# Performance work log

Measured on AMD Instinct MI355X. Metric: run time of the kernel, lower is better.

Reference implementation:

```python
import jax, jax.numpy as jnp
import numpy as np

S = 2048        # tokens (single prefill sequence)
HID = 3584      # hidden_size
H = 16          # num query heads
KV = 8          # num kv heads
D = 256         # head_dim
WINDOW = 1024   # sliding window size
CAP = 50.0      # logit softcap
SCALE = 256.0 ** -0.5   # query_pre_attn_scalar ** -0.5
THETA = 10000.0


def setup_inputs() -> dict:
    key = jax.random.key(0)
    ks = jax.random.split(key, 5)
    hidden_states = jax.random.normal(ks[0], (S, HID), dtype=jnp.float32)
    positions = jnp.arange(S, dtype=jnp.int32)
    Wq = jax.random.normal(ks[1], (HID, H * D), dtype=jnp.float32) * 0.02
    Wk = jax.random.normal(ks[2], (HID, KV * D), dtype=jnp.float32) * 0.02
    Wv = jax.random.normal(ks[3], (HID, KV * D), dtype=jnp.float32) * 0.02
    Wo = jax.random.normal(ks[4], (H * D, HID), dtype=jnp.float32) * 0.02
    return {"hidden_states": hidden_states, "positions": positions,
            "Wq": Wq, "Wk": Wk, "Wv": Wv, "Wo": Wo}


def _rope_neox(x, positions):
    # x: [S, n_heads, D]; neox-style: rotate halves, full rotary_dim == D
    half = D // 2
    inv_freq = 1.0 / (THETA ** (jnp.arange(0, half, dtype=jnp.float32) * 2.0 / D))
    freqs = positions.astype(jnp.float32)[:, None] * inv_freq[None, :]  # [S, half]
    cos = jnp.cos(freqs)[:, None, :].astype(x.dtype)
    sin = jnp.sin(freqs)[:, None, :].astype(x.dtype)
    x1, x2 = x[..., :half], x[..., half:]
    return jnp.concatenate([x1 * cos - x2 * sin, x2 * cos + x1 * sin], axis=-1)


def reference(hidden_states, positions, Wq, Wk, Wv, Wo):
    # QKV projections (no bias)
    q = (hidden_states @ Wq).reshape(S, H, D)
    k = (hidden_states @ Wk).reshape(S, KV, D)
    v = (hidden_states @ Wv).reshape(S, KV, D)
    q = _rope_neox(q, positions)
    k = _rope_neox(k, positions)
    # grouped-query attention: G query heads per kv head
    G = H // KV
    qg = q.reshape(S, KV, G, D)
    scores = jnp.einsum('qkgd,skd->kgqs', qg, k) * jnp.asarray(SCALE, q.dtype)
    # logit soft-capping
    scores = CAP * jnp.tanh(scores / CAP)
    # causal + sliding-window mask
    i = positions[:, None]
    j = positions[None, :]
    mask = (j <= i) & ((i - j) < WINDOW)   # [S, S]
    neg = jnp.finfo(scores.dtype).min
    scores = jnp.where(mask[None, None, :, :], scores, neg)
    p = jax.nn.softmax(scores, axis=-1)
    attn = jnp.einsum('kgqs,skd->qkgd', p, v).reshape(S, H * D)
    return attn @ Wo
```

## Files before the change

### kernel.cpp

```cpp
#include <hip/hip_runtime.h>
#include <stdint.h>

#define S 2048
#define HID 3584
#define NH 16
#define NKV 8
#define DH 256
#define WINDOW 1024
#define SCALE 0.0625f
#define CAP 50.0f

typedef short s16x8 __attribute__((ext_vector_type(8)));
typedef float f32x4 __attribute__((ext_vector_type(4)));

__device__ __forceinline__ short f2bf(float f) {
  union { float f; uint32_t u; } c; c.f = f;
  uint32_t u = c.u;
  uint32_t r = (u + 0x7FFFu + ((u >> 16) & 1u)) >> 16;
  return (short)r;
}
__device__ __forceinline__ float bf2f(short s) {
  union { uint32_t u; float f; } c;
  c.u = ((uint32_t)(uint16_t)s) << 16;
  return c.f;
}
__device__ __forceinline__ void gll16(const void* g, void* l) {
  __builtin_amdgcn_global_load_lds((const __attribute__((address_space(1))) void*)g,
                                   (__attribute__((address_space(3))) void*)l, 16, 0, 0);
}
#define BAR() asm volatile("s_barrier" ::: "memory")
#define VW6() asm volatile("s_waitcnt vmcnt(6)" ::: "memory")

__global__ void rope_table_kernel(float2* __restrict__ tbl) {
  int idx = blockIdx.x * 256 + threadIdx.x;
  int s = idx >> 7, i = idx & 127;
  float inv = __expf(-(float)i * (9.210340371976184f / 128.0f));
  float fr = (float)s * inv;
  tbl[idx] = make_float2(cosf(fr), sinf(fr));
}

__global__ void conv_hs_kernel(const float* __restrict__ src, short* __restrict__ dst) {
  int gid = blockIdx.x * 256 + threadIdx.x;
  float4 a = *(const float4*)&src[(size_t)gid * 8];
  float4 b = *(const float4*)&src[(size_t)gid * 8 + 4];
  s16x8 o;
  o[0] = f2bf(a.x); o[1] = f2bf(a.y); o[2] = f2bf(a.z); o[3] = f2bf(a.w);
  o[4] = f2bf(b.x); o[5] = f2bf(b.y); o[6] = f2bf(b.z); o[7] = f2bf(b.w);
  *(s16x8*)&dst[(size_t)gid * 8] = o;
}

__global__ __launch_bounds__(256)
void transpose_kernel(const float* __restrict__ src, short* __restrict__ dst,
                      int K, int N)
{
  __shared__ __align__(16) short t[64][76];
  int ntn = N >> 6;
  int tn = blockIdx.x % ntn, tk = blockIdx.x / ntn;
  int tid = threadIdx.x;
  int c = tid & 63, rg = tid >> 6;
  #pragma unroll
  for (int i = 0; i < 4; ++i) {
    int r0 = i * 16 + rg * 4;
    short tmp[4];
    #pragma unroll
    for (int j = 0; j < 4; ++j)
      tmp[j] = f2bf(src[(size_t)(tk * 64 + r0 + j) * N + tn * 64 + c]);
    *(short4*)&t[c][r0] = *(short4*)tmp;
  }
  __syncthreads();
  #pragma unroll
  for (int it = 0; it < 2; ++it) {
    int flat = it * 256 + tid;
    int n = flat >> 3, kc = flat & 7;
    *(s16x8*)&dst[(size_t)(tn * 64 + n) * K + tk * 64 + kc * 8] = *(s16x8*)&t[n][kc * 8];
  }
}

template<int BN, int KS>
__device__ __forceinline__ void gemm_ph(const short* __restrict__ srcA,
                                        const short* __restrict__ srcB,
                                        int tid, int NT,
                                        f32x4 (&acc)[8][BN / 64])
{
  constexpr int NFP = BN / 128;
  constexpr int BTILE = BN * 64;
  __shared__ __align__(16) short Asb[2 * 16384];
  __shared__ __align__(16) short Bsb[2 * BTILE];
  const int wv = tid >> 6, lane = tid & 63;
  const int lr = lane & 15, lk = lane >> 4;
  const int wm_id = wv >> 2, wn_id = wv & 3;
  const int r7 = lr & 7;
  const int abase = (wm_id * 128 + lr) * 64 + ((lk ^ r7) * 8);
  const int bbase = (wn_id * (BN / 4) + lr) * 64 + ((lk ^ r7) * 8);

  s16x8 af[4][2];
  s16x8 bfr[2][NFP][2];

  auto stA = [&](int ts, int r, int b) {
    gll16(srcA + (size_t)ts * 64 + (size_t)(r * 64) * KS,
          Asb + b * 16384 + r * 4096 + wv * 512);
  };
  auto stB = [&](int ts, int q, int b) {
    gll16(srcB + (size_t)ts * 64 + (size_t)(q * 64) * KS,
          Bsb + b * BTILE + q * 4096 + wv * 512);
  };
  auto LDA = [&](int mh, int b) {
    const short* A = Asb + b * 16384;
    #pragma unroll
    for (int mf = 0; mf < 4; ++mf)
      #pragma unroll
      for (int kh = 0; kh < 2; ++kh)
        af[mf][kh] = *(const s16x8*)&A[(abase + (mh * 64 + mf * 16) * 64) ^ (kh * 32)];
  };
  auto LDB = [&](int nh, int b) {
    const short* B = Bsb + b * BTILE;
    #pragma unroll
    for (int nf = 0; nf < NFP; ++nf)
      #pragma unroll
      for (int kh = 0; kh < 2; ++kh)
        bfr[nh][nf][kh] = *(const s16x8*)&B[(bbase + (nh * NFP + nf) * 16 * 64) ^ (kh * 32)];
  };
  auto MMA = [&](int mh, int nh) {
    asm volatile("s_waitcnt lgkmcnt(0)" ::: "memory");
    __builtin_amdgcn_sched_barrier(0);
    __builtin_amdgcn_s_setprio(1);
    #pragma unroll
    for (int mf = 0; mf < 4; ++mf)
      #pragma unroll
      for (int nf = 0; nf < NFP; ++nf) {
        acc[mh * 4 + mf][nh * NFP + nf] =
          __builtin_amdgcn_mfma_f32_16x16x32_bf16(af[mf][0], bfr[nh][nf][0],
                                                  acc[mh * 4 + mf][nh * NFP + nf], 0, 0, 0);
        acc[mh * 4 + mf][nh * NFP + nf] =
          __builtin_amdgcn_mfma_f32_16x16x32_bf16(af[mf][1], bfr[nh][nf][1],
                                                  acc[mh * 4 + mf][nh * NFP + nf], 0, 0, 0);
      }
    __builtin_amdgcn_s_setprio(0);
  };

  #pragma unroll
  for (int r = 0; r < 4; ++r) stA(0, r, 0);
  #pragma unroll
  for (int q = 0; q < BN / 64; ++q) stB(0, q, 0);
  #pragma unroll
  for (int r = 0; r < 4; ++r) stA(1, r, 1);
  if constexpr (BN == 256) { stB(1, 0, 1); stB(1, 1, 1); }
  else                     { stB(1, 0, 1); stB(1, 1, 1); }
  asm volatile("s_waitcnt vmcnt(0)" ::: "memory");
  BAR();

  const int NI = NT / 2;
  for (int i = 0; i < NI; ++i) {
    const int T = 2 * i;
    const int t2 = (T + 2 < NT) ? T + 2 : NT - 2;
    const int t3 = (T + 3 < NT) ? T + 3 : NT - 1;
    LDA(0, 0); LDB(0, 0);
    if constexpr (BN == 256) { stB(T + 1, 2, 1); stB(T + 1, 3, 1); }
    BAR(); MMA(0, 0); BAR();
    LDB(1, 0);
    stA(t2, 0, 0); stA(t2, 2, 0);
    BAR(); MMA(0, 1); BAR();
    LDA(1, 0);
    stB(t2, 0, 0); stB(t2, 1, 0);
    BAR(); MMA(1, 0); BAR();
    stA(t2, 1, 0); stA(t2, 3, 0);
    VW6();
    BAR(); MMA(1, 1); BAR();
    LDA(0, 1); LDB(0, 1);
    if constexpr (BN == 256) { stB(t2, 2, 0); stB(t2, 3, 0); }
    BAR(); MMA(0, 0); BAR();
    LDB(1, 1);
    stA(t3, 0, 1); stA(t3, 2, 1);
    BAR(); MMA(0, 1); BAR();
    LDA(1, 1);
    stB(t3, 0, 1); stB(t3, 1, 1);
    BAR(); MMA(1, 0); BAR();
    stA(t3, 1, 1); stA(t3, 3, 1);
    VW6();
    BAR(); MMA(1, 1); BAR();
  }
  asm volatile("s_waitcnt vmcnt(0)" ::: "memory");
}

__global__ __launch_bounds__(512, 2)
void qkv_gemm8_kernel(const short* __restrict__ hsb, const short* __restrict__ Wt,
                      short* __restrict__ qb, short* __restrict__ kbuf,
                      short* __restrict__ vtb)
{
  int bid = blockIdx.x;
  int swz = (bid & 7) * 32 + (bid >> 3);
  int bm = swz >> 5, bn = swz & 31;
  int m0 = bm * 256, n0 = bn * 256;
  int tid = threadIdx.x;
  int row8 = tid >> 3;
  int colsw = ((tid & 7) ^ (row8 & 7)) * 8;
  const short* srcA = hsb + (size_t)(m0 + row8) * HID + colsw;
  const short* srcB = Wt + (size_t)(n0 + row8) * HID + colsw;
  f32x4 acc[8][4] = {};
  gemm_ph<256, HID>(srcA, srcB, tid, HID / 64, acc);

  int wv = tid >> 6, lane = tid & 63;
  int lr = lane & 15, lk = lane >> 4;
  int wm = (wv >> 2) * 128, wn = (wv & 3) * 64;
  int region = (n0 < 4096) ? 0 : ((n0 < 6144) ? 1 : 2);
  #pragma unroll
  for (int m = 0; m < 8; ++m) {
    int srow_b = m0 + wm + m * 16 + lk * 4;
    #pragma unroll
    for (int n = 0; n < 4; ++n) {
      int ncol = n0 + wn + n * 16 + lr;
      #pragma unroll
      for (int r = 0; r < 4; ++r) {
        int srow = srow_b + r;
        short bv = f2bf(acc[m][n][r]);
        if (region == 0) {
          int h = ncol >> 8, d = ncol & 255;
          qb[((size_t)h * S + srow) * DH + d] = bv;
        } else if (region == 1) {
          int c = ncol - 4096; int kv = c >> 8, d = c & 255;
          kbuf[((size_t)kv * S + srow) * DH + d] = bv;
        } else {
          int c = ncol - 6144; int kv = c >> 8, d = c & 255;
          vtb[((size_t)kv * DH + d) * S + srow] = bv;
        }
      }
    }
  }
}

__global__ __launch_bounds__(512, 2)
void out_gemm8_kernel(const short* __restrict__ attnb, const short* __restrict__ WtO,
                      float* __restrict__ out)
{
  int bid = blockIdx.x;
  int swz = (bid & 7) * 28 + (bid >> 3);
  int bm = swz / 28, bn = swz % 28;
  int m0 = bm * 256, n0 = bn * 128;
  int tid = threadIdx.x;
  int row8 = tid >> 3;
  int colsw = ((tid & 7) ^ (row8 & 7)) * 8;
  const short* srcA = attnb + (size_t)(m0 + row8) * 4096 + colsw;
  const short* srcB = WtO + (size_t)(n0 + row8) * 4096 + colsw;
  f32x4 acc[8][2] = {};
  gemm_ph<128, 4096>(srcA, srcB, tid, 4096 / 64, acc);

  int wv = tid >> 6, lane = tid & 63;
  int lr = lane & 15, lk = lane >> 4;
  int wm = (wv >> 2) * 128, wn = (wv & 3) * 32;
  #pragma unroll
  for (int m = 0; m < 8; ++m) {
    int srow_b = m0 + wm + m * 16 + lk * 4;
    #pragma unroll
    for (int n = 0; n < 2; ++n) {
      int ncol = n0 + wn + n * 16 + lr;
      #pragma unroll
      for (int r = 0; r < 4; ++r)
        out[(size_t)(srow_b + r) * HID + ncol] = acc[m][n][r];
    }
  }
}

__global__ void rope_kernel(short* __restrict__ qb, short* __restrict__ kbuf,
                            const float2* __restrict__ tbl)
{
  int gid = blockIdx.x * 256 + threadIdx.x;
  int row = gid >> 4, ch = gid & 15;
  short* base = (row < NH * S) ? (qb + (size_t)row * DH)
                               : (kbuf + (size_t)(row - NH * S) * DH);
  int s = row & (S - 1);
  int i0 = ch * 8;
  s16x8 x1 = *(s16x8*)(base + i0);
  s16x8 x2 = *(s16x8*)(base + 128 + i0);
  s16x8 y1, y2;
  #pragma unroll
  for (int j = 0; j < 8; ++j) {
    float2 cs = tbl[s * 128 + i0 + j];
    float a = bf2f(x1[j]), b = bf2f(x2[j]);
    y1[j] = f2bf(a * cs.x - b * cs.y);
    y2[j] = f2bf(b * cs.x + a * cs.y);
  }
  *(s16x8*)(base + i0) = y1;
  *(s16x8*)(base + 128 + i0) = y2;
}

__global__ __launch_bounds__(256)
void attn_kernel(const short* __restrict__ qb, const short* __restrict__ kbuf,
                 const short* __restrict__ vtb, short* __restrict__ attnb)
{
  __shared__ __align__(16) short Klds[64][264];
  __shared__ __align__(16) short Vlds[256][72];
  __shared__ __align__(16) short Plds[4][16][72];
  int bid = blockIdx.x;
  int h = bid >> 5, qt = bid & 31;
  int kv = h >> 1;
  int q0 = qt * 64;
  int tid = threadIdx.x, w = tid >> 6, lane = tid & 63;
  int lr = lane & 15, lk = lane >> 4;
  int qrow_base = q0 + w * 16;
  s16x8 qf[8];
  const short* qrow = qb + ((size_t)h * S + (qrow_base + lr)) * DH;
  #pragma unroll
  for (int kb = 0; kb < 8; ++kb)
    qf[kb] = *(const s16x8*)(qrow + kb * 32 + lk * 8);
  f32x4 acc_o[16] = {};
  float m_r[4], l_r[4];
  #pragma unroll
  for (int r = 0; r < 4; ++r) { m_r[r] = -1e30f; l_r[r] = 0.0f; }
  int tlo = (q0 >= WINDOW - 1) ? ((q0 - (WINDOW - 1)) >> 6) : 0;
  int thi = q0 >> 6;
  const short* kbase = kbuf + (size_t)kv * S * DH;
  const short* vbase = vtb + (size_t)kv * DH * S;
  for (int t = tlo; t <= thi; ++t) {
    int k0 = t * 64;
    __syncthreads();
    #pragma unroll
    for (int it = 0; it < 8; ++it) {
      int ch = it * 256 + tid;
      int r = ch >> 5, cg = ch & 31;
      *(s16x8*)&Klds[r][cg * 8] = *(const s16x8*)(kbase + (size_t)(k0 + r) * DH + cg * 8);
    }
    #pragma unroll
    for (int it = 0; it < 8; ++it) {
      int ch = it * 256 + tid;
      int r = ch >> 3, cg = ch & 7;
      *(s16x8*)&Vlds[r][cg * 8] = *(const s16x8*)(vbase + (size_t)r * S + k0 + cg * 8);
    }
    __syncthreads();
    f32x4 sc[4] = {};
    #pragma unroll
    for (int kb = 0; kb < 8; ++kb)
      #pragma unroll
      for (int ni = 0; ni < 4; ++ni) {
        s16x8 b = *(const s16x8*)&Klds[ni * 16 + lr][kb * 32 + lk * 8];
        sc[ni] = __builtin_amdgcn_mfma_f32_16x16x32_bf16(qf[kb], b, sc[ni], 0, 0, 0);
      }
    bool validm[4][4];
    #pragma unroll
    for (int ni = 0; ni < 4; ++ni)
      #pragma unroll
      for (int r = 0; r < 4; ++r) {
        float sv = sc[ni][r] * SCALE;
        sv = CAP * tanhf(sv * (1.0f / CAP));
        int qg = qrow_base + lk * 4 + r;
        int kg = k0 + ni * 16 + lr;
        bool valid = (kg <= qg) && (qg - kg < WINDOW);
        validm[ni][r] = valid;
        sc[ni][r] = valid ? sv : -1e30f;
      }
    float alpha[4];
    #pragma unroll
    for (int r = 0; r < 4; ++r) {
      float mx = fmaxf(fmaxf(sc[0][r], sc[1][r]), fmaxf(sc[2][r], sc[3][r]));
      #pragma unroll
      for (int off = 1; off < 16; off <<= 1)
        mx = fmaxf(mx, __shfl_xor(mx, off, 64));
      float mnew = fmaxf(m_r[r], mx);
      alpha[r] = __expf(m_r[r] - mnew);
      m_r[r] = mnew;
      float sum = 0.0f;
      #pragma unroll
      for (int ni = 0; ni < 4; ++ni) {
        float p = validm[ni][r] ? __expf(sc[ni][r] - mnew) : 0.0f;
        sc[ni][r] = p;
        sum += p;
      }
      #pragma unroll
      for (int off = 1; off < 16; off <<= 1)
        sum += __shfl_xor(sum, off, 64);
      l_r[r] = l_r[r] * alpha[r] + sum;
    }
    #pragma unroll
    for (int ni = 0; ni < 4; ++ni)
      #pragma unroll
      for (int r = 0; r < 4; ++r)
        Plds[w][lk * 4 + r][ni * 16 + lr] = f2bf(sc[ni][r]);
    __syncthreads();
    #pragma unroll
    for (int df = 0; df < 16; ++df)
      #pragma unroll
      for (int r = 0; r < 4; ++r)
        acc_o[df][r] *= alpha[r];
    s16x8 pa0 = *(const s16x8*)&Plds[w][lr][lk * 8];
    s16x8 pa1 = *(const s16x8*)&Plds[w][lr][32 + lk * 8];
    #pragma unroll
    for (int df = 0; df < 16; ++df) {
      s16x8 b0 = *(const s16x8*)&Vlds[df * 16 + lr][lk * 8];
      s16x8 b1 = *(const s16x8*)&Vlds[df * 16 + lr][32 + lk * 8];
      acc_o[df] = __builtin_amdgcn_mfma_f32_16x16x32_bf16(pa0, b0, acc_o[df], 0, 0, 0);
      acc_o[df] = __builtin_amdgcn_mfma_f32_16x16x32_bf16(pa1, b1, acc_o[df], 0, 0, 0);
    }
  }
  #pragma unroll
  for (int r = 0; r < 4; ++r) {
    int srow = qrow_base + lk * 4 + r;
    float inv = 1.0f / l_r[r];
    #pragma unroll
    for (int df = 0; df < 16; ++df)
      attnb[(size_t)srow * (NH * DH) + h * DH + df * 16 + lr] = f2bf(acc_o[df][r] * inv);
  }
}

extern "C" void kernel_launch(void* const* d_in, const int* in_sizes, int n_in,
                              void* d_out, int out_size, void* d_ws, size_t ws_size,
                              hipStream_t stream) {
  const float* hs = (const float*)d_in[0];
  const float* Wq = (const float*)d_in[2];
  const float* Wk = (const float*)d_in[3];
  const float* Wv = (const float*)d_in[4];
  const float* Wo = (const float*)d_in[5];
  float* out = (float*)d_out;
  char* ws = (char*)d_ws;
  size_t off = 0;
  float2* tbl  = (float2*)(ws + off); off += 2097152;
  short* qb    = (short*)(ws + off);  off += 16777216;
  short* kbuf  = (short*)(ws + off);  off += 8388608;
  short* vtb   = (short*)(ws + off);  off += 8388608;
  short* attnb = (short*)(ws + off);  off += 16777216;
  short* hsb   = (short*)(ws + off);  off += 14680064;
  short* Wt    = (short*)(ws + off);  off += 58720256;
  short* WtO   = (short*)(ws + off);  off += 29360128;

  hipLaunchKernelGGL(rope_table_kernel, dim3(1024), dim3(256), 0, stream, tbl);
  hipLaunchKernelGGL(conv_hs_kernel, dim3(3584), dim3(256), 0, stream, hs, hsb);
  hipLaunchKernelGGL(transpose_kernel, dim3(64 * 56), dim3(256), 0, stream,
                     Wq, Wt, HID, 4096);
  hipLaunchKernelGGL(transpose_kernel, dim3(32 * 56), dim3(256), 0, stream,
                     Wk, Wt + (size_t)4096 * HID, HID, 2048);
  hipLaunchKernelGGL(transpose_kernel, dim3(32 * 56), dim3(256), 0, stream,
                     Wv, Wt + (size_t)6144 * HID, HID, 2048);
  hipLaunchKernelGGL(transpose_kernel, dim3(56 * 64), dim3(256), 0, stream,
                     Wo, WtO, 4096, HID);
  hipLaunchKernelGGL(qkv_gemm8_kernel, dim3(256), dim3(512), 0, stream,
                     hsb, Wt, qb, kbuf, vtb);
  hipLaunchKernelGGL(rope_kernel, dim3(3072), dim3(256), 0, stream, qb, kbuf, tbl);
  hipLaunchKernelGGL(attn_kernel, dim3(512), dim3(256), 0, stream,
                     qb, kbuf, vtb, attnb);
  hipLaunchKernelGGL(out_gemm8_kernel, dim3(224), dim3(512), 0, stream,
                     attnb, WtO, out);
}
```

Measured before the change: 444.3 us.

## Stream V from global, swizzle K LDS, reorder blocks, fast tanh

```diff
diff --git a/kernel.cpp b/kernel.cpp
--- a/kernel.cpp
+++ b/kernel.cpp
@@ -144,8 +144,7 @@
   for (int q = 0; q < BN / 64; ++q) stB(0, q, 0);
   #pragma unroll
   for (int r = 0; r < 4; ++r) stA(1, r, 1);
-  if constexpr (BN == 256) { stB(1, 0, 1); stB(1, 1, 1); }
-  else                     { stB(1, 0, 1); stB(1, 1, 1); }
+  stB(1, 0, 1); stB(1, 1, 1);
   asm volatile("s_waitcnt vmcnt(0)" ::: "memory");
   BAR();
 
@@ -287,11 +286,10 @@
 void attn_kernel(const short* __restrict__ qb, const short* __restrict__ kbuf,
                  const short* __restrict__ vtb, short* __restrict__ attnb)
 {
-  __shared__ __align__(16) short Klds[64][264];
-  __shared__ __align__(16) short Vlds[256][72];
+  __shared__ __align__(16) short Klds[64][256];
   __shared__ __align__(16) short Plds[4][16][72];
   int bid = blockIdx.x;
-  int h = bid >> 5, qt = bid & 31;
+  int qt = bid >> 4, h = bid & 15;
   int kv = h >> 1;
   int q0 = qt * 64;
   int tid = threadIdx.x, w = tid >> 6, lane = tid & 63;
@@ -317,30 +315,29 @@
     for (int it = 0; it < 8; ++it) {
       int ch = it * 256 + tid;
       int r = ch >> 5, cg = ch & 31;
-      *(s16x8*)&Klds[r][cg * 8] = *(const s16x8*)(kbase + (size_t)(k0 + r) * DH + cg * 8);
-    }
-    #pragma unroll
-    for (int it = 0; it < 8; ++it) {
-      int ch = it * 256 + tid;
-      int r = ch >> 3, cg = ch & 7;
-      *(s16x8*)&Vlds[r][cg * 8] = *(const s16x8*)(vbase + (size_t)r * S + k0 + cg * 8);
+      *(s16x8*)&Klds[r][(cg ^ (r & 7)) * 8] =
+        *(const s16x8*)(kbase + (size_t)(k0 + r) * DH + cg * 8);
     }
     __syncthreads();
     f32x4 sc[4] = {};
+    __builtin_amdgcn_s_setprio(1);
     #pragma unroll
     for (int kb = 0; kb < 8; ++kb)
       #pragma unroll
       for (int ni = 0; ni < 4; ++ni) {
-        s16x8 b = *(const s16x8*)&Klds[ni * 16 + lr][kb * 32 + lk * 8];
+        int row = ni * 16 + lr;
+        s16x8 b = *(const s16x8*)&Klds[row][(((kb << 2) | lk) ^ (row & 7)) * 8];
         sc[ni] = __builtin_amdgcn_mfma_f32_16x16x32_bf16(qf[kb], b, sc[ni], 0, 0, 0);
       }
+    __builtin_amdgcn_s_setprio(0);
     bool validm[4][4];
     #pragma unroll
     for (int ni = 0; ni < 4; ++ni)
       #pragma unroll
       for (int r = 0; r < 4; ++r) {
         float sv = sc[ni][r] * SCALE;
-        sv = CAP * tanhf(sv * (1.0f / CAP));
+        float e = __expf(sv * (2.0f / CAP));
+        sv = CAP * __fdividef(e - 1.0f, e + 1.0f);
         int qg = qrow_base + lk * 4 + r;
         int kg = k0 + ni * 16 + lr;
         bool valid = (kg <= qg) && (qg - kg < WINDOW);
@@ -374,7 +371,6 @@
       #pragma unroll
       for (int r = 0; r < 4; ++r)
         Plds[w][lk * 4 + r][ni * 16 + lr] = f2bf(sc[ni][r]);
-    __syncthreads();
     #pragma unroll
     for (int df = 0; df < 16; ++df)
       #pragma unroll
@@ -382,13 +378,17 @@
         acc_o[df][r] *= alpha[r];
     s16x8 pa0 = *(const s16x8*)&Plds[w][lr][lk * 8];
     s16x8 pa1 = *(const s16x8*)&Plds[w][lr][32 + lk * 8];
+    const short* vcol = vbase + k0 + lk * 8;
+    __builtin_amdgcn_s_setprio(1);
     #pragma unroll
     for (int df = 0; df < 16; ++df) {
-      s16x8 b0 = *(const s16x8*)&Vlds[df * 16 + lr][lk * 8];
-      s16x8 b1 = *(const s16x8*)&Vlds[df * 16 + lr][32 + lk * 8];
+      const short* vr = vcol + (size_t)(df * 16 + lr) * S;
+      s16x8 b0 = *(const s16x8*)vr;
+      s16x8 b1 = *(const s16x8*)(vr + 32);
       acc_o[df] = __builtin_amdgcn_mfma_f32_16x16x32_bf16(pa0, b0, acc_o[df], 0, 0, 0);
       acc_o[df] = __builtin_amdgcn_mfma_f32_16x16x32_bf16(pa1, b1, acc_o[df], 0, 0, 0);
     }
+    __builtin_amdgcn_s_setprio(0);
   }
   #pragma unroll
   for (int r = 0; r < 4; ++r) {
```

Result: slower. 457.7 us (+3.0%).
